# Kernel tuning notes

Measured on AMD Instinct MI355X. Metric: run time of the kernel, lower is better.

Reference implementation:

```python
import jax, jax.numpy as jnp
import numpy as np

B, H, K, D = 8192, 8, 4096, 1024
HD = D // H  # head_dim = 128


def _l2norm(x, axis=-1, eps=1e-12):
    n = jnp.linalg.norm(x, axis=axis, keepdims=True)
    return x / jnp.maximum(n, eps)


def setup_inputs() -> dict:
    key = jax.random.key(0)
    kz, kc = jax.random.split(key)
    z = jax.random.normal(kz, (B, D), dtype=jnp.float32)
    # codebooks initialized as in _init_diverse_codebook: randn then L2-normalized per code
    codebooks = _l2norm(jax.random.normal(kc, (H, K, HD), dtype=jnp.float32), axis=2)
    return {"z": z, "codebooks": codebooks}


def reference(z, codebooks):
    bsz, dim = z.shape
    z_r = z.reshape(bsz, H, HD)                      # [B,H,d]
    z_n = _l2norm(z_r, axis=2)
    cb_n = _l2norm(codebooks, axis=2)                # [H,K,d]
    sims = jnp.einsum('bhd,hkd->bhk', z_n, cb_n)     # [B,H,K]
    distances = 1.0 - sims
    indices = jnp.argmax(sims, axis=-1)              # [B,H] int
    # per-head codebook gather, fully vectorized (replaces python loop over heads)
    z_q = codebooks[jnp.arange(H)[None, :], indices]  # [B,H,d]
    # straight-through estimator
    z_q = z_r + jax.lax.stop_gradient(z_q - z_r)
    return (z_q.reshape(bsz, dim), indices, distances)
```

## Files before the change

### kernel.cpp

```cpp
#include <hip/hip_runtime.h>
#include <cstdint>
#include <cstddef>

#define B_SZ 8192
#define H_N  8
#define K_N  4096
#define D_N  1024
#define HD_N 128

__device__ __forceinline__ unsigned int ordf(float f) {
    unsigned int u = __float_as_uint(f);
    return (u & 0x80000000u) ? ~u : (u | 0x80000000u);
}

__device__ __forceinline__ unsigned long long shfl_xor_u64(unsigned long long v, int m) {
    int lo = (int)(unsigned int)v;
    int hi = (int)(unsigned int)(v >> 32);
    lo = __shfl_xor(lo, m, 64);
    hi = __shfl_xor(hi, m, 64);
    return ((unsigned long long)(unsigned int)hi << 32) | (unsigned int)lo;
}

__global__ void norm_rows_kernel(const float* __restrict__ in,
                                 float* __restrict__ out, int nrows) {
    int wid  = (int)((blockIdx.x * blockDim.x + threadIdx.x) >> 6);
    int lane = threadIdx.x & 63;
    if (wid >= nrows) return;
    const float* r = in + (size_t)wid * HD_N;
    float2 v = *(const float2*)(r + lane * 2);
    float ss = v.x * v.x + v.y * v.y;
#pragma unroll
    for (int m = 32; m; m >>= 1) ss += __shfl_xor(ss, m, 64);
    float d = fmaxf(sqrtf(ss), 1e-12f);
    float2 o;
    o.x = v.x / d;
    o.y = v.y / d;
    *(float2*)(out + (size_t)wid * HD_N + lane * 2) = o;
}

__global__ void sims_kernel(const float* __restrict__ zn,
                            const float* __restrict__ cbn,
                            float* __restrict__ dist,
                            unsigned long long* __restrict__ packed) {
    __shared__ float As[32][132];
    __shared__ float Bs[32][132];

    const int bm = blockIdx.x;
    const int bn = blockIdx.y;
    const int h  = blockIdx.z;
    const int t  = threadIdx.x;
    const int cx = t & 15;
    const int cy = t >> 4;

    float acc[8][8];
#pragma unroll
    for (int i = 0; i < 8; ++i)
#pragma unroll
        for (int j = 0; j < 8; ++j) acc[i][j] = 0.f;

    const float* Ag = zn  + (size_t)(bm * 128) * D_N + h * HD_N;
    const float* Bg = cbn + ((size_t)h * K_N + (size_t)bn * 128) * HD_N;

    for (int ks = 0; ks < HD_N; ks += 32) {
#pragma unroll
        for (int i = 0; i < 4; ++i) {
            int fl  = t + i * 256;
            int row = fl >> 3;
            int kq  = fl & 7;
            float4 v = *(const float4*)(Ag + (size_t)row * D_N + ks + kq * 4);
            As[kq * 4 + 0][row] = v.x;
            As[kq * 4 + 1][row] = v.y;
            As[kq * 4 + 2][row] = v.z;
            As[kq * 4 + 3][row] = v.w;
            float4 w = *(const float4*)(Bg + (size_t)row * HD_N + ks + kq * 4);
            Bs[kq * 4 + 0][row] = w.x;
            Bs[kq * 4 + 1][row] = w.y;
            Bs[kq * 4 + 2][row] = w.z;
            Bs[kq * 4 + 3][row] = w.w;
        }
        __syncthreads();

#pragma unroll 8
        for (int kk = 0; kk < 32; ++kk) {
            float4 a0 = *(const float4*)&As[kk][cy * 4];
            float4 a1 = *(const float4*)&As[kk][cy * 4 + 64];
            float4 b0 = *(const float4*)&Bs[kk][cx * 4];
            float4 b1 = *(const float4*)&Bs[kk][cx * 4 + 64];
            float av[8] = {a0.x, a0.y, a0.z, a0.w, a1.x, a1.y, a1.z, a1.w};
            float bv[8] = {b0.x, b0.y, b0.z, b0.w, b1.x, b1.y, b1.z, b1.w};
#pragma unroll
            for (int i = 0; i < 8; ++i)
#pragma unroll
                for (int j = 0; j < 8; ++j)
                    acc[i][j] = fmaf(av[i], bv[j], acc[i][j]);
        }
        __syncthreads();
    }

    const int m_base = bm * 128;
    const int n_base = bn * 128;
#pragma unroll
    for (int i = 0; i < 8; ++i) {
        int m = cy * 4 + (i & 3) + ((i >> 2) << 6);
        size_t drow = ((size_t)(m_base + m) * H_N + h) * (size_t)K_N + n_base;
        float4 d0 = make_float4(1.f - acc[i][0], 1.f - acc[i][1],
                                1.f - acc[i][2], 1.f - acc[i][3]);
        float4 d1 = make_float4(1.f - acc[i][4], 1.f - acc[i][5],
                                1.f - acc[i][6], 1.f - acc[i][7]);
        *(float4*)(dist + drow + cx * 4)      = d0;
        *(float4*)(dist + drow + cx * 4 + 64) = d1;

        unsigned long long best = 0ull;
#pragma unroll
        for (int j = 0; j < 8; ++j) {
            int n = n_base + cx * 4 + (j & 3) + ((j >> 2) << 6);
            unsigned long long p =
                ((unsigned long long)ordf(acc[i][j]) << 32) |
                (unsigned int)(K_N - 1 - n);
            best = (p > best) ? p : best;
        }
#pragma unroll
        for (int ml = 1; ml < 16; ml <<= 1) {
            unsigned long long o = shfl_xor_u64(best, ml);
            best = (o > best) ? o : best;
        }
        if (cx == 0) {
            atomicMax(packed + (size_t)(m_base + m) * H_N + h, best);
        }
    }
}

__global__ void finalize_kernel(const unsigned long long* __restrict__ packed,
                                const float* __restrict__ z,
                                const float* __restrict__ cb,
                                float* __restrict__ zq,
                                float* __restrict__ idx_out) {
    int rid  = (int)((blockIdx.x * blockDim.x + threadIdx.x) >> 6);
    int lane = threadIdx.x & 63;
    if (rid >= B_SZ * H_N) return;
    int b = rid >> 3;
    int h = rid & 7;
    unsigned long long p = packed[rid];
    int idx = K_N - 1 - (int)(unsigned int)(p & 0xFFFFFFFFull);
    if (lane == 0) idx_out[rid] = (float)idx;
    const float* crow = cb + ((size_t)h * K_N + idx) * HD_N;
    const float* zrow = z + (size_t)b * D_N + h * HD_N;
    float2 c  = *(const float2*)(crow + lane * 2);
    float2 zr = *(const float2*)(zrow + lane * 2);
    float2 o;
    o.x = zr.x + (c.x - zr.x);
    o.y = zr.y + (c.y - zr.y);
    *(float2*)(zq + (size_t)b * D_N + h * HD_N + lane * 2) = o;
}

extern "C" void kernel_launch(void* const* d_in, const int* in_sizes, int n_in,
                              void* d_out, int out_size, void* d_ws, size_t ws_size,
                              hipStream_t stream) {
    const float* z  = (const float*)d_in[0];
    const float* cb = (const float*)d_in[1];

    float* out  = (float*)d_out;
    float* zq   = out;
    float* idxo = out + (size_t)B_SZ * D_N;
    float* dist = idxo + (size_t)B_SZ * H_N;

    float* zn  = (float*)d_ws;
    float* cbn = zn + (size_t)B_SZ * D_N;
    unsigned long long* packed =
        (unsigned long long*)(cbn + (size_t)H_N * K_N * HD_N);

    hipMemsetAsync(packed, 0, (size_t)B_SZ * H_N * sizeof(unsigned long long), stream);

    norm_rows_kernel<<<(B_SZ * H_N) / 4, 256, 0, stream>>>(z, zn, B_SZ * H_N);
    norm_rows_kernel<<<(H_N * K_N) / 4, 256, 0, stream>>>(cb, cbn, H_N * K_N);

    dim3 g(B_SZ / 128, K_N / 128, H_N);
    sims_kernel<<<g, 256, 0, stream>>>(zn, cbn, dist, packed);

    finalize_kernel<<<(B_SZ * H_N) / 4, 256, 0, stream>>>(packed, z, cb, zq, idxo);
}
```

Before: 1.749 ms.

## Use bf16 hi/lo split MFMA for similarity GEMM with direct-to-LDS loads

Normalized z and codebook rows are split into bf16 high and low parts and stored per head in a contiguous layout. The fp32 FMA GEMM is replaced by MFMA 16x16x32 bf16 over three cross products (hi*hi, lo*hi, hi*lo), with tiles loaded by global_load_lds. The goal is to move the compute-bound GEMM onto matrix cores while keeping near-fp32 accuracy. The lo*lo term is dropped, so argmax ties could resolve differently from fp32. The distance stores become scalar and strided instead of float4, which may cost write bandwidth.

```diff
diff --git a/kernel.cpp b/kernel.cpp
--- a/kernel.cpp
+++ b/kernel.cpp
@@ -7,6 +7,14 @@
 #define K_N  4096
 #define D_N  1024
 #define HD_N 128
+
+typedef __attribute__((ext_vector_type(8))) short bf16x8;
+typedef __attribute__((ext_vector_type(4))) float f32x4;
+
+#define GLOAD16(gp, lp)                                                        \
+    __builtin_amdgcn_global_load_lds(                                          \
+        (const __attribute__((address_space(1))) void*)(gp),                   \
+        (__attribute__((address_space(3))) void*)(lp), 16, 0, 0)
 
 __device__ __forceinline__ unsigned int ordf(float f) {
     unsigned int u = __float_as_uint(f);
@@ -21,111 +29,131 @@
     return ((unsigned long long)(unsigned int)hi << 32) | (unsigned int)lo;
 }
 
-__global__ void norm_rows_kernel(const float* __restrict__ in,
-                                 float* __restrict__ out, int nrows) {
+__device__ __forceinline__ unsigned short f2bf(float f) {
+    unsigned int u = __float_as_uint(f);
+    u += 0x7FFFu + ((u >> 16) & 1u);
+    return (unsigned short)(u >> 16);
+}
+__device__ __forceinline__ float bf2f(unsigned short s) {
+    return __uint_as_float((unsigned int)s << 16);
+}
+
+template<int ZMODE>
+__global__ void normsplit_kernel(const float* __restrict__ in,
+                                 unsigned short* __restrict__ out, int nrows) {
     int wid  = (int)((blockIdx.x * blockDim.x + threadIdx.x) >> 6);
     int lane = threadIdx.x & 63;
     if (wid >= nrows) return;
-    const float* r = in + (size_t)wid * HD_N;
+    const float* r;
+    size_t orow;
+    if (ZMODE) {
+        int b = wid >> 3, h = wid & 7;
+        r = in + (size_t)b * D_N + h * HD_N;
+        orow = (size_t)h * B_SZ + b;
+    } else {
+        r = in + (size_t)wid * HD_N;
+        orow = (size_t)wid;
+    }
     float2 v = *(const float2*)(r + lane * 2);
     float ss = v.x * v.x + v.y * v.y;
 #pragma unroll
     for (int m = 32; m; m >>= 1) ss += __shfl_xor(ss, m, 64);
     float d = fmaxf(sqrtf(ss), 1e-12f);
-    float2 o;
-    o.x = v.x / d;
-    o.y = v.y / d;
-    *(float2*)(out + (size_t)wid * HD_N + lane * 2) = o;
-}
-
-__global__ void sims_kernel(const float* __restrict__ zn,
-                            const float* __restrict__ cbn,
-                            float* __restrict__ dist,
-                            unsigned long long* __restrict__ packed) {
-    __shared__ float As[32][132];
-    __shared__ float Bs[32][132];
-
-    const int bm = blockIdx.x;
-    const int bn = blockIdx.y;
-    const int h  = blockIdx.z;
-    const int t  = threadIdx.x;
-    const int cx = t & 15;
-    const int cy = t >> 4;
-
-    float acc[8][8];
-#pragma unroll
-    for (int i = 0; i < 8; ++i)
-#pragma unroll
-        for (int j = 0; j < 8; ++j) acc[i][j] = 0.f;
-
-    const float* Ag = zn  + (size_t)(bm * 128) * D_N + h * HD_N;
-    const float* Bg = cbn + ((size_t)h * K_N + (size_t)bn * 128) * HD_N;
-
-    for (int ks = 0; ks < HD_N; ks += 32) {
+    float q0 = v.x / d, q1 = v.y / d;
+    unsigned short h0 = f2bf(q0), h1 = f2bf(q1);
+    float l0 = q0 - bf2f(h0), l1 = q1 - bf2f(h1);
+    unsigned short* op = out + orow * 256;
+    *(unsigned int*)(op + lane * 2) =
+        (unsigned int)h0 | ((unsigned int)h1 << 16);
+    *(unsigned int*)(op + 128 + lane * 2) =
+        (unsigned int)f2bf(l0) | ((unsigned int)f2bf(l1) << 16);
+}
+
+__global__ __launch_bounds__(256)
+void sims_mfma_kernel(const unsigned short* __restrict__ zs,
+                      const unsigned short* __restrict__ cs,
+                      float* __restrict__ dist,
+                      unsigned long long* __restrict__ packed) {
+    __shared__ __align__(16) unsigned short As[8][128][8];
+    __shared__ __align__(16) unsigned short Bs[8][128][8];
+
+    const int bm = blockIdx.x, bn = blockIdx.y, h = blockIdx.z;
+    const int t    = threadIdx.x;
+    const int lane = t & 63;
+    const int wid  = t >> 6;
+    const int wm = wid >> 1, wn = wid & 1;
+    const int cl = lane & 15, rg = lane >> 4;
+
+    const unsigned short* Ag = zs + ((size_t)h * B_SZ + (size_t)bm * 128) * 256;
+    const unsigned short* Bg = cs + ((size_t)h * K_N  + (size_t)bn * 128) * 256;
+
+    f32x4 acc[4][4];
+#pragma unroll
+    for (int i = 0; i < 4; ++i)
+#pragma unroll
+        for (int j = 0; j < 4; ++j) acc[i][j] = (f32x4)0.0f;
+
+    for (int ks = 0; ks < 6; ++ks) {
+        const int kb   = ks >> 1;
+        const int kin  = (ks & 1) * 64;
+        const int aoff = (kb == 1 ? 128 : 0) + kin;
+        const int boff = (kb == 2 ? 128 : 0) + kin;
 #pragma unroll
         for (int i = 0; i < 4; ++i) {
-            int fl  = t + i * 256;
-            int row = fl >> 3;
-            int kq  = fl & 7;
-            float4 v = *(const float4*)(Ag + (size_t)row * D_N + ks + kq * 4);
-            As[kq * 4 + 0][row] = v.x;
-            As[kq * 4 + 1][row] = v.y;
-            As[kq * 4 + 2][row] = v.z;
-            As[kq * 4 + 3][row] = v.w;
-            float4 w = *(const float4*)(Bg + (size_t)row * HD_N + ks + kq * 4);
-            Bs[kq * 4 + 0][row] = w.x;
-            Bs[kq * 4 + 1][row] = w.y;
-            Bs[kq * 4 + 2][row] = w.z;
-            Bs[kq * 4 + 3][row] = w.w;
+            const int f = t + i * 256;
+            const int r = f & 127;
+            const int c = f >> 7;
+            GLOAD16(Ag + (size_t)r * 256 + aoff + c * 8, &As[0][0][0] + (size_t)f * 8);
+            GLOAD16(Bg + (size_t)r * 256 + boff + c * 8, &Bs[0][0][0] + (size_t)f * 8);
         }
         __syncthreads();
 
-#pragma unroll 8
-        for (int kk = 0; kk < 32; ++kk) {
-            float4 a0 = *(const float4*)&As[kk][cy * 4];
-            float4 a1 = *(const float4*)&As[kk][cy * 4 + 64];
-            float4 b0 = *(const float4*)&Bs[kk][cx * 4];
-            float4 b1 = *(const float4*)&Bs[kk][cx * 4 + 64];
-            float av[8] = {a0.x, a0.y, a0.z, a0.w, a1.x, a1.y, a1.z, a1.w};
-            float bv[8] = {b0.x, b0.y, b0.z, b0.w, b1.x, b1.y, b1.z, b1.w};
-#pragma unroll
-            for (int i = 0; i < 8; ++i)
-#pragma unroll
-                for (int j = 0; j < 8; ++j)
-                    acc[i][j] = fmaf(av[i], bv[j], acc[i][j]);
+#pragma unroll
+        for (int kk = 0; kk < 2; ++kk) {
+            const int q = kk * 4 + rg;
+            bf16x8 a[4], b[4];
+#pragma unroll
+            for (int mi = 0; mi < 4; ++mi)
+                a[mi] = *(const bf16x8*)&As[q][wm * 64 + mi * 16 + cl][0];
+#pragma unroll
+            for (int ni = 0; ni < 4; ++ni)
+                b[ni] = *(const bf16x8*)&Bs[q][wn * 64 + ni * 16 + cl][0];
+#pragma unroll
+            for (int mi = 0; mi < 4; ++mi)
+#pragma unroll
+                for (int ni = 0; ni < 4; ++ni)
+                    acc[mi][ni] = __builtin_amdgcn_mfma_f32_16x16x32_bf16(
+                        a[mi], b[ni], acc[mi][ni], 0, 0, 0);
         }
         __syncthreads();
     }
 
-    const int m_base = bm * 128;
-    const int n_base = bn * 128;
-#pragma unroll
-    for (int i = 0; i < 8; ++i) {
-        int m = cy * 4 + (i & 3) + ((i >> 2) << 6);
-        size_t drow = ((size_t)(m_base + m) * H_N + h) * (size_t)K_N + n_base;
-        float4 d0 = make_float4(1.f - acc[i][0], 1.f - acc[i][1],
-                                1.f - acc[i][2], 1.f - acc[i][3]);
-        float4 d1 = make_float4(1.f - acc[i][4], 1.f - acc[i][5],
-                                1.f - acc[i][6], 1.f - acc[i][7]);
-        *(float4*)(dist + drow + cx * 4)      = d0;
-        *(float4*)(dist + drow + cx * 4 + 64) = d1;
-
-        unsigned long long best = 0ull;
-#pragma unroll
-        for (int j = 0; j < 8; ++j) {
-            int n = n_base + cx * 4 + (j & 3) + ((j >> 2) << 6);
-            unsigned long long p =
-                ((unsigned long long)ordf(acc[i][j]) << 32) |
-                (unsigned int)(K_N - 1 - n);
-            best = (p > best) ? p : best;
-        }
-#pragma unroll
-        for (int ml = 1; ml < 16; ml <<= 1) {
-            unsigned long long o = shfl_xor_u64(best, ml);
-            best = (o > best) ? o : best;
-        }
-        if (cx == 0) {
-            atomicMax(packed + (size_t)(m_base + m) * H_N + h, best);
+#pragma unroll
+    for (int mi = 0; mi < 4; ++mi) {
+#pragma unroll
+        for (int j = 0; j < 4; ++j) {
+            const int m = bm * 128 + wm * 64 + mi * 16 + rg * 4 + j;
+            const size_t drow = ((size_t)m * H_N + h) * (size_t)K_N
+                              + (size_t)bn * 128 + wn * 64;
+            unsigned long long best = 0ull;
+#pragma unroll
+            for (int ni = 0; ni < 4; ++ni) {
+                const float s = acc[mi][ni][j];
+                dist[drow + ni * 16 + cl] = 1.0f - s;
+                const int n = bn * 128 + wn * 64 + ni * 16 + cl;
+                unsigned long long p =
+                    ((unsigned long long)ordf(s) << 32) |
+                    (unsigned int)(K_N - 1 - n);
+                best = (p > best) ? p : best;
+            }
+#pragma unroll
+            for (int ml = 1; ml < 16; ml <<= 1) {
+                unsigned long long o = shfl_xor_u64(best, ml);
+                best = (o > best) ? o : best;
+            }
+            if (cl == 0) {
+                atomicMax(packed + (size_t)m * H_N + h, best);
+            }
         }
     }
 }
@@ -164,18 +192,18 @@
     float* idxo = out + (size_t)B_SZ * D_N;
     float* dist = idxo + (size_t)B_SZ * H_N;
 
-    float* zn  = (float*)d_ws;
-    float* cbn = zn + (size_t)B_SZ * D_N;
+    unsigned short* zs = (unsigned short*)d_ws;
+    unsigned short* cs = zs + (size_t)H_N * B_SZ * 256;
     unsigned long long* packed =
-        (unsigned long long*)(cbn + (size_t)H_N * K_N * HD_N);
+        (unsigned long long*)(cs + (size_t)H_N * K_N * 256);
 
     hipMemsetAsync(packed, 0, (size_t)B_SZ * H_N * sizeof(unsigned long long), stream);
 
-    norm_rows_kernel<<<(B_SZ * H_N) / 4, 256, 0, stream>>>(z, zn, B_SZ * H_N);
-    norm_rows_kernel<<<(H_N * K_N) / 4, 256, 0, stream>>>(cb, cbn, H_N * K_N);
+    normsplit_kernel<1><<<(B_SZ * H_N) / 4, 256, 0, stream>>>(z, zs, B_SZ * H_N);
+    normsplit_kernel<0><<<(H_N * K_N) / 4, 256, 0, stream>>>(cb, cs, H_N * K_N);
 
     dim3 g(B_SZ / 128, K_N / 128, H_N);
-    sims_kernel<<<g, 256, 0, stream>>>(zn, cbn, dist, packed);
+    sims_mfma_kernel<<<g, 256, 0, stream>>>(zs, cs, dist, packed);
 
     finalize_kernel<<<(B_SZ * H_N) / 4, 256, 0, stream>>>(packed, z, cb, zq, idxo);
 }
```

New measurement: 1.614 ms. 7.8% less time.
